# Kernel optimization log

Measured on AMD Instinct MI355X. Metric: run time of the kernel, lower is better.

Reference implementation:

```python
import jax, jax.numpy as jnp
import numpy as np

B, C, H, W = 4, 64, 160, 160
COUT, K = 64, 3
STRIDE, PAD, DIL = 1, 1, 1


def setup_inputs() -> dict:
    key = jax.random.key(0)
    k1, k2, k3, k4, k5 = jax.random.split(key, 5)
    x = jax.random.normal(k1, (B, C, H, W), dtype=jnp.float32)
    # small offset-conv weights -> offsets of O(1) pixel, realistic sampling
    w_off = jax.random.normal(k2, (2 * K * K, C, K, K), dtype=jnp.float32) * 0.01
    b_off = jax.random.normal(k3, (2 * K * K,), dtype=jnp.float32) * 0.01
    weight = jax.random.normal(k4, (COUT, C, K, K), dtype=jnp.float32) / np.sqrt(C * K * K)
    bias = jax.random.normal(k5, (COUT,), dtype=jnp.float32) * 0.01
    return {"x": x, "w_off": w_off, "b_off": b_off, "weight": weight, "bias": bias}


def _deform_conv2d(x, offset, weight, bias):
    """torchvision-style deform_conv2d (v1, groups=1, offset_groups=1)."""
    b, c, h, w = x.shape
    cout, _, k, _ = weight.shape
    kk = k * k
    ho, wo = offset.shape[2], offset.shape[3]
    off = offset.reshape(b, kk, 2, ho, wo)
    dy, dx = off[:, :, 0], off[:, :, 1]  # [B,KK,Ho,Wo]
    # base sampling grid: p0 + kernel offset
    base_y = (jnp.arange(ho) * STRIDE - PAD)[None, :] + (jnp.arange(k) * DIL)[:, None]  # [K,Ho]
    base_x = (jnp.arange(wo) * STRIDE - PAD)[None, :] + (jnp.arange(k) * DIL)[:, None]  # [K,Wo]
    by = jnp.repeat(base_y, k, axis=0)   # [KK,Ho]  (k index = kh*K + kw)
    bx = jnp.tile(base_x, (k, 1))        # [KK,Wo]
    py = by[None, :, :, None] + dy       # [B,KK,Ho,Wo]
    px = bx[None, :, None, :] + dx
    y0 = jnp.floor(py)
    x0 = jnp.floor(px)
    ly = (py - y0)[:, None]              # [B,1,KK,Ho,Wo]
    lx = (px - x0)[:, None]
    y0i = y0.astype(jnp.int32)
    x0i = x0.astype(jnp.int32)
    x_flat = x.reshape(b, c, h * w)

    def gather(yi, xi):
        valid = (yi >= 0) & (yi < h) & (xi >= 0) & (xi < w)
        yc = jnp.clip(yi, 0, h - 1)
        xc = jnp.clip(xi, 0, w - 1)
        lin = (yc * w + xc).reshape(b, 1, -1)
        v = jnp.take_along_axis(x_flat, lin, axis=2).reshape(b, c, kk, ho, wo)
        return v * valid[:, None].astype(x.dtype)

    v00 = gather(y0i, x0i)
    v01 = gather(y0i, x0i + 1)
    v10 = gather(y0i + 1, x0i)
    v11 = gather(y0i + 1, x0i + 1)
    sampled = (v00 * (1 - ly) * (1 - lx) + v01 * (1 - ly) * lx
               + v10 * ly * (1 - lx) + v11 * ly * lx)  # [B,C,KK,Ho,Wo]
    out = jnp.einsum('bckhw,ock->bohw', sampled, weight.reshape(cout, c, kk))
    return out + bias[None, :, None, None]


def reference(x, w_off, b_off, weight, bias):
    offset = jax.lax.conv_general_dilated(
        x, w_off, (STRIDE, STRIDE), ((PAD, PAD), (PAD, PAD)),
        rhs_dilation=(DIL, DIL),
        dimension_numbers=('NCHW', 'OIHW', 'NCHW')) + b_off[None, :, None, None]
    return _deform_conv2d(x, offset, weight, bias)
```

## Files before the change

kernel.cpp:

```cpp
#include <hip/hip_runtime.h>
#include <hip/hip_bf16.h>

#define Bq   4
#define Cc   64
#define Hh   160
#define Ww   160
#define HWp  (Hh * Ww)
#define COUTc 64

typedef __attribute__((ext_vector_type(8))) _Float16 f16x8;
typedef __attribute__((ext_vector_type(4))) _Float16 f16x4;
typedef __attribute__((ext_vector_type(4))) float f32x4;
typedef __attribute__((ext_vector_type(2))) float f32x2;
typedef __attribute__((ext_vector_type(4))) int   int4v;

#define WTBF_SHORTS   (72 * 512)
#define WTOFFF_SHORTS (36 * 512)
#define XCL_OFS       (WTBF_SHORTS + WTOFFF_SHORTS)
#define XCL_PIX       ((size_t)Bq * HWp)
#define XCL_SHORTS    (XCL_PIX * 64 + 64)

#define HROWS 6
#define HCOLS 36
#define HPX   72
#define HSTR  (HCOLS * HPX)

__device__ __forceinline__ short f2h(float f) {
    union { _Float16 h; short s; } v; v.h = (_Float16)f; return v.s;
}
__device__ __forceinline__ unsigned pk2h(float a, float b) {
    union { _Float16 h[2]; unsigned u; } v;
    v.h[0] = (_Float16)a; v.h[1] = (_Float16)b; return v.u;
}
__device__ __forceinline__ f16x8 vsplat(_Float16 v) {
    return (f16x8){v, v, v, v, v, v, v, v};
}

__global__ __launch_bounds__(256) void prep_all(const float* __restrict__ x,
                                                const float* __restrict__ w,
                                                const float* __restrict__ w_off,
                                                short* __restrict__ ws) {
    int blk = blockIdx.x;
    int tid = threadIdx.x;
    if (blk < 400) {
        int g = blk * 256 + tid;
        int b = g / HWp, p = g - b * HWp;
        const float* xp = x + (size_t)b * Cc * HWp + p;
        short* op = ws + XCL_OFS + (size_t)g * 64;
#pragma unroll
        for (int cg = 0; cg < 8; ++cg) {
            unsigned d[4];
#pragma unroll
            for (int dj = 0; dj < 4; ++dj) {
                float f0 = xp[(size_t)(cg * 8 + 2 * dj) * HWp];
                float f1 = xp[(size_t)(cg * 8 + 2 * dj + 1) * HWp];
                d[dj] = pk2h(f0, f1);
            }
            *(int4v*)(op + cg * 8) = *(int4v*)d;
        }
    } else if (blk < 544) {
        int i = (blk - 400) * 256 + tid;
        if (i < WTBF_SHORTS) {
            int fidx = i >> 9, r = i & 511;
            int l = r >> 3, j = r & 7;
            int cg = fidx & 3, th = fidx >> 2;
            int tap = th >> 1, h = th & 1;
            int o = cg * 16 + (l & 15);
            int c = h * 32 + ((l >> 4) << 3) + j;
            ws[i] = f2h(w[o * 576 + c * 9 + tap]);
        }
        if (i < WTOFFF_SHORTS) {
            int fidx = i >> 9, r = i & 511;
            int l = r >> 3, j = r & 7;
            int g = fidx & 1, th = fidx >> 1;
            int tap = th >> 1, h = th & 1;
            int oc = g * 16 + (l & 15);
            int c = h * 32 + ((l >> 4) << 3) + j;
            float v = (oc < 18) ? w_off[oc * 576 + c * 9 + tap] : 0.f;
            ws[WTBF_SHORTS + i] = f2h(v);
        }
    } else {
        if (tid < 8)
            *(int4v*)((char*)(ws + XCL_OFS) + XCL_PIX * 128 + tid * 16) =
                (int4v){0, 0, 0, 0};
    }
}

__global__ __launch_bounds__(256, 4) void fused_cl(const short* __restrict__ ws,
                                                   const float* __restrict__ b_off,
                                                   const float* __restrict__ bias,
                                                   float* __restrict__ out) {
    __shared__ short halo_s[HROWS * HCOLS * HPX];
    __shared__ float offbuf[32][20];
    __shared__ int4v tapT[32][9];

    int tid = threadIdx.x;
    int wid = tid >> 6;
    int l   = tid & 63;
    int lr  = l & 15;
    int lg  = l >> 4;
    int mhalf = wid >> 1;
    int nhalf = wid & 1;

    int bid = blockIdx.x;
    int g_blk = (bid & 7) * 400 + (bid >> 3);

    int pix_base = g_blk * 32;
    int b   = pix_base / HWp;
    int rem = pix_base - b * HWp;
    int y   = rem / Ww;
    int x0  = rem - y * Ww;

    const short* wTbF   = ws;
    const short* wToffF = ws + WTBF_SHORTS;
    const char*  xclb   = (const char*)(ws + XCL_OFS) + (size_t)b * HWp * 128;

    for (int i = tid; i < HROWS * HCOLS * 8; i += 256) {
        int pl = i >> 3, cg2 = i & 7;
        int hy = pl / HCOLS, hx = pl - hy * HCOLS;
        int gy = y - 2 + hy, gx = x0 - 2 + hx;
        int4v v;
        if (gy >= 0 && gy < Hh && gx >= 0 && gx < Ww)
            v = *(const int4v*)(xclb + (size_t)(gy * Ww + gx) * 128 + cg2 * 16);
        else
            v = (int4v){0, 0, 0, 0};
        *(int4v*)(halo_s + pl * HPX + cg2 * 8) = v;
    }
    __syncthreads();

    {
        int hxb = mhalf * 16 + lr + 1;
        int hoffA[9];
#pragma unroll
        for (int t = 0; t < 9; ++t) {
            int ty = t / 3, tx = t - ty * 3;
            hoffA[t] = (ty + 1) * HSTR + (hxb + tx) * HPX + lg * 8;
        }
        const short* wofr = wToffF + (size_t)nhalf * 512 + l * 8;
        f32x4 accA = {0.f, 0.f, 0.f, 0.f};
        f32x4 accB = {0.f, 0.f, 0.f, 0.f};
        f16x8 sB[4];
#pragma unroll
        for (int u = 0; u < 4; ++u)
            sB[u] = *(const f16x8*)(wofr + u * 1024);
        f16x8 sa2[2];
        sa2[0] = *(const f16x8*)(halo_s + hoffA[0]);
#pragma unroll
        for (int u = 0; u < 18; ++u) {
            const int s = u & 3;
            if (u + 1 < 18) {
                const int t2 = (u + 1) >> 1, h2 = (u + 1) & 1;
                sa2[(u + 1) & 1] = *(const f16x8*)(halo_s + hoffA[t2] + h2 * 32);
            }
            if (u & 1)
                accB = __builtin_amdgcn_mfma_f32_16x16x32_f16(sa2[u & 1], sB[s], accB, 0, 0, 0);
            else
                accA = __builtin_amdgcn_mfma_f32_16x16x32_f16(sa2[u & 1], sB[s], accA, 0, 0, 0);
            if (u + 4 < 18)
                sB[s] = *(const f16x8*)(wofr + (u + 4) * 1024);
            __builtin_amdgcn_sched_barrier(0);
        }
        int oc_row = nhalf * 16 + lr;
        if (oc_row < 18) {
            float bv = b_off[oc_row];
#pragma unroll
            for (int j = 0; j < 4; ++j)
                offbuf[mhalf * 16 + lg * 4 + j][oc_row] = accA[j] + accB[j] + bv;
        }
    }
    __syncthreads();

    for (int i = tid; i < 288; i += 256) {
        int px = i / 9, tap = i - px * 9;
        int ty = tap / 3, tx = tap - ty * 3;
        f32x2 d2 = *(const f32x2*)&offbuf[px][2 * tap];
        float py  = (float)(y - 1 + ty) + d2[0];
        float pxf = (float)(x0 + px - 1 + tx) + d2[1];
        float fy = floorf(py), fx = floorf(pxf);
        float ly = py - fy, lx = pxf - fx;
        int iy0 = (int)fy, ix0 = (int)fx;
        int iy1 = iy0 + 1, ix1 = ix0 + 1;
        bool vy0 = (iy0 >= 0) && (iy0 < Hh);
        bool vy1 = (iy1 >= 0) && (iy1 < Hh);
        bool vx0 = (ix0 >= 0) && (ix0 < Ww);
        bool vx1 = (ix1 >= 0) && (ix1 < Ww);
        float w00 = (vy0 && vx0) ? (1.f - ly) * (1.f - lx) : 0.f;
        float w01 = (vy0 && vx1) ? (1.f - ly) * lx         : 0.f;
        float w10 = (vy1 && vx0) ? ly * (1.f - lx)         : 0.f;
        float w11 = (vy1 && vx1) ? ly * lx                 : 0.f;
        int hy = iy0 - (y - 2);
        int hx = ix0 - (x0 - 2);
        bool inH = (hy >= 0) && (hy <= HROWS - 2) && (hx >= 0) && (hx <= HCOLS - 2);
        union { f16x4 h4; int iw[2]; } wu;
        wu.h4 = (f16x4){(_Float16)w00, (_Float16)w01,
                        (_Float16)w10, (_Float16)w11};
        int4v tv;
        tv[0] = inH ? (hy * HSTR + hx * HPX) : -1;
        tv[1] = (iy0 & 0xffff) | (ix0 << 16);
        tv[2] = wu.iw[0];
        tv[3] = wu.iw[1];
        tapT[px][tap] = tv;
    }
    __syncthreads();

    f32x4 acc[2];
    acc[0] = (f32x4){0.f, 0.f, 0.f, 0.f};
    acc[1] = (f32x4){0.f, 0.f, 0.f, 0.f};
    int px_t = mhalf * 16 + lr;
    const short* wfb = wTbF + (size_t)nhalf * 1024 + l * 8;

    f16x8 sB0[2], sB1[2];
    sB0[0] = *(const f16x8*)(wfb);
    sB1[0] = *(const f16x8*)(wfb + 512);
    sB0[1] = *(const f16x8*)(wfb + 2048);
    sB1[1] = *(const f16x8*)(wfb + 2048 + 512);

    int4v tp[2];
    tp[0] = tapT[px_t][0];
    tp[1] = tapT[px_t][1];

    f16x8 cst[2][8];
    {
        const short* q = halo_s + max(tp[0][0], 0) + lg * 8;
#pragma unroll
        for (int h = 0; h < 2; ++h) {
            const short* qh = q + h * 32;
            cst[0][h * 4 + 0] = *(const f16x8*)(qh);
            cst[0][h * 4 + 1] = *(const f16x8*)(qh + HPX);
            cst[0][h * 4 + 2] = *(const f16x8*)(qh + HSTR);
            cst[0][h * 4 + 3] = *(const f16x8*)(qh + HSTR + HPX);
        }
    }

#pragma unroll
    for (int t = 0; t < 9; ++t) {
        const int cur = t & 1, nx = cur ^ 1;

        const int ho = tp[cur][0];
        const int fb = tp[cur][1];
        union { int iw[2]; f16x4 h4; } wu;
        wu.iw[0] = tp[cur][2];
        wu.iw[1] = tp[cur][3];
        f16x4 wg = wu.h4;

        if (t + 2 < 9)
            tp[cur] = tapT[px_t][t + 2];

        if (t < 8) {
            const short* q = halo_s + max(tp[nx][0], 0) + lg * 8;
#pragma unroll
            for (int h = 0; h < 2; ++h) {
                const short* qh = q + h * 32;
                cst[nx][h * 4 + 0] = *(const f16x8*)(qh);
                cst[nx][h * 4 + 1] = *(const f16x8*)(qh + HPX);
                cst[nx][h * 4 + 2] = *(const f16x8*)(qh + HSTR);
                cst[nx][h * 4 + 3] = *(const f16x8*)(qh + HSTR + HPX);
            }
        }
        __builtin_amdgcn_sched_barrier(0);

#pragma unroll
        for (int h = 0; h < 2; ++h) {
            const int u = 2 * t + h, s = u & 1;
            f16x8 a = cst[cur][h * 4 + 0] * vsplat(wg[0])
                    + cst[cur][h * 4 + 1] * vsplat(wg[1])
                    + cst[cur][h * 4 + 2] * vsplat(wg[2])
                    + cst[cur][h * 4 + 3] * vsplat(wg[3]);
            if (ho < 0) {
                int iy0 = (int)(short)(fb & 0xffff);
                int ix0 = fb >> 16;
                int cy0 = min(max(iy0, 0), Hh - 1), cy1 = min(max(iy0 + 1, 0), Hh - 1);
                int cx0 = min(max(ix0, 0), Ww - 1), cx1 = min(max(ix0 + 1, 0), Ww - 1);
                int cbh = h * 64 + lg * 16;
                f16x8 g00 = *(const f16x8*)(xclb + (size_t)(cy0 * Ww + cx0) * 128 + cbh);
                f16x8 g01 = *(const f16x8*)(xclb + (size_t)(cy0 * Ww + cx1) * 128 + cbh);
                f16x8 g10 = *(const f16x8*)(xclb + (size_t)(cy1 * Ww + cx0) * 128 + cbh);
                f16x8 g11 = *(const f16x8*)(xclb + (size_t)(cy1 * Ww + cx1) * 128 + cbh);
                a = g00 * vsplat(wg[0]) + g01 * vsplat(wg[1])
                  + g10 * vsplat(wg[2]) + g11 * vsplat(wg[3]);
            }
            acc[0] = __builtin_amdgcn_mfma_f32_16x16x32_f16(a, sB0[s], acc[0], 0, 0, 0);
            acc[1] = __builtin_amdgcn_mfma_f32_16x16x32_f16(a, sB1[s], acc[1], 0, 0, 0);
            if (u + 2 < 18) {
                sB0[s] = *(const f16x8*)(wfb + (u + 2) * 2048);
                sB1[s] = *(const f16x8*)(wfb + (u + 2) * 2048 + 512);
            }
        }
        __builtin_amdgcn_sched_barrier(0);
    }

    float* obase = out + (size_t)b * COUTc * HWp + y * Ww + x0;
#pragma unroll
    for (int nt = 0; nt < 2; ++nt) {
        int o = nhalf * 32 + nt * 16 + lr;
        float bv = bias[o];
#pragma unroll
        for (int j = 0; j < 4; ++j)
            obase[(size_t)o * HWp + mhalf * 16 + lg * 4 + j] = acc[nt][j] + bv;
    }
}

extern "C" void kernel_launch(void* const* d_in, const int* in_sizes, int n_in,
                              void* d_out, int out_size, void* d_ws, size_t ws_size,
                              hipStream_t stream) {
    const float* x      = (const float*)d_in[0];
    const float* w_off  = (const float*)d_in[1];
    const float* b_off  = (const float*)d_in[2];
    const float* weight = (const float*)d_in[3];
    const float* bias   = (const float*)d_in[4];
    float* outp = (float*)d_out;
    short* ws   = (short*)d_ws;

    prep_all<<<545, 256, 0, stream>>>(x, weight, w_off, ws);

    int nblocks = (Bq * HWp) / 32;
    fused_cl<<<nblocks, 256, 0, stream>>>(ws, b_off, bias, outp);
}
```

Baseline: 53.06 us.

## Process 2x32 pixel tiles per block with each wave covering all output channels

Each block now handles two output rows of 32 pixels instead of one row, so the halo grows from 6 to 7 rows and is shared by twice as many pixels, which cuts the halo-load overhead per pixel. Each wave now computes 16 pixels across all 64 output channels (and both offset-channel tiles) rather than splitting channels between waves. This removes the duplicated bilinear sampling work that the old channel split caused. The costs are more registers per thread, more LDS per block, and a lower occupancy hint (3 blocks instead of 4). The block count is halved and the grid index swizzle is adjusted to match.

Result: faster. 49.65 us (median of 3 runs) (-6.4%).

```diff
diff --git a/kernel.cpp b/kernel.cpp
--- a/kernel.cpp
+++ b/kernel.cpp
@@ -20,7 +20,7 @@
 #define XCL_PIX       ((size_t)Bq * HWp)
 #define XCL_SHORTS    (XCL_PIX * 64 + 64)
 
-#define HROWS 6
+#define HROWS 7
 #define HCOLS 36
 #define HPX   72
 #define HSTR  (HCOLS * HPX)
@@ -86,30 +86,29 @@
     }
 }
 
-__global__ __launch_bounds__(256, 4) void fused_cl(const short* __restrict__ ws,
+__global__ __launch_bounds__(256, 3) void fused_cl(const short* __restrict__ ws,
                                                    const float* __restrict__ b_off,
                                                    const float* __restrict__ bias,
                                                    float* __restrict__ out) {
     __shared__ short halo_s[HROWS * HCOLS * HPX];
-    __shared__ float offbuf[32][20];
-    __shared__ int4v tapT[32][9];
+    __shared__ float offbuf[64][20];
+    __shared__ int4v tapT[64][9];
 
     int tid = threadIdx.x;
     int wid = tid >> 6;
     int l   = tid & 63;
     int lr  = l & 15;
     int lg  = l >> 4;
-    int mhalf = wid >> 1;
-    int nhalf = wid & 1;
 
     int bid = blockIdx.x;
-    int g_blk = (bid & 7) * 400 + (bid >> 3);
-
-    int pix_base = g_blk * 32;
-    int b   = pix_base / HWp;
-    int rem = pix_base - b * HWp;
-    int y   = rem / Ww;
-    int x0  = rem - y * Ww;
+    int g_blk = (bid & 7) * 200 + (bid >> 3);
+
+    int b  = g_blk / 400;
+    int r  = g_blk - b * 400;
+    int ty2 = r / 5;
+    int tx2 = r - ty2 * 5;
+    int y  = ty2 * 2;
+    int x0 = tx2 * 32;
 
     const short* wTbF   = ws;
     const short* wToffF = ws + WTBF_SHORTS;
@@ -129,53 +128,61 @@
     __syncthreads();
 
     {
-        int hxb = mhalf * 16 + lr + 1;
+        int rowoff = wid >> 1;
+        int colw   = (wid & 1) * 16 + lr;
+        int hxb    = colw + 1;
         int hoffA[9];
 #pragma unroll
         for (int t = 0; t < 9; ++t) {
             int ty = t / 3, tx = t - ty * 3;
-            hoffA[t] = (ty + 1) * HSTR + (hxb + tx) * HPX + lg * 8;
-        }
-        const short* wofr = wToffF + (size_t)nhalf * 512 + l * 8;
-        f32x4 accA = {0.f, 0.f, 0.f, 0.f};
-        f32x4 accB = {0.f, 0.f, 0.f, 0.f};
-        f16x8 sB[4];
-#pragma unroll
-        for (int u = 0; u < 4; ++u)
-            sB[u] = *(const f16x8*)(wofr + u * 1024);
+            hoffA[t] = (rowoff + ty + 1) * HSTR + (hxb + tx) * HPX + lg * 8;
+        }
+        const short* wofr = wToffF + l * 8;
+        f32x4 accO0 = {0.f, 0.f, 0.f, 0.f};
+        f32x4 accO1 = {0.f, 0.f, 0.f, 0.f};
+        f16x8 sB0[4], sB1[4];
+#pragma unroll
+        for (int u = 0; u < 4; ++u) {
+            sB0[u] = *(const f16x8*)(wofr + u * 1024);
+            sB1[u] = *(const f16x8*)(wofr + u * 1024 + 512);
+        }
         f16x8 sa2[2];
         sa2[0] = *(const f16x8*)(halo_s + hoffA[0]);
 #pragma unroll
         for (int u = 0; u < 18; ++u) {
-            const int s = u & 3;
+            const int s4 = u & 3;
             if (u + 1 < 18) {
                 const int t2 = (u + 1) >> 1, h2 = (u + 1) & 1;
                 sa2[(u + 1) & 1] = *(const f16x8*)(halo_s + hoffA[t2] + h2 * 32);
             }
-            if (u & 1)
-                accB = __builtin_amdgcn_mfma_f32_16x16x32_f16(sa2[u & 1], sB[s], accB, 0, 0, 0);
-            else
-                accA = __builtin_amdgcn_mfma_f32_16x16x32_f16(sa2[u & 1], sB[s], accA, 0, 0, 0);
-            if (u + 4 < 18)
-                sB[s] = *(const f16x8*)(wofr + (u + 4) * 1024);
+            accO0 = __builtin_amdgcn_mfma_f32_16x16x32_f16(sa2[u & 1], sB0[s4], accO0, 0, 0, 0);
+            accO1 = __builtin_amdgcn_mfma_f32_16x16x32_f16(sa2[u & 1], sB1[s4], accO1, 0, 0, 0);
+            if (u + 4 < 18) {
+                sB0[s4] = *(const f16x8*)(wofr + (u + 4) * 1024);
+                sB1[s4] = *(const f16x8*)(wofr + (u + 4) * 1024 + 512);
+            }
             __builtin_amdgcn_sched_barrier(0);
         }
-        int oc_row = nhalf * 16 + lr;
-        if (oc_row < 18) {
-            float bv = b_off[oc_row];
+        float bv0 = b_off[lr];
+#pragma unroll
+        for (int j = 0; j < 4; ++j)
+            offbuf[wid * 16 + lg * 4 + j][lr] = accO0[j] + bv0;
+        if (lr < 2) {
+            float bv1 = b_off[16 + lr];
 #pragma unroll
             for (int j = 0; j < 4; ++j)
-                offbuf[mhalf * 16 + lg * 4 + j][oc_row] = accA[j] + accB[j] + bv;
+                offbuf[wid * 16 + lg * 4 + j][16 + lr] = accO1[j] + bv1;
         }
     }
     __syncthreads();
 
-    for (int i = tid; i < 288; i += 256) {
+    for (int i = tid; i < 576; i += 256) {
         int px = i / 9, tap = i - px * 9;
+        int prow = px >> 5, pcol = px & 31;
         int ty = tap / 3, tx = tap - ty * 3;
         f32x2 d2 = *(const f32x2*)&offbuf[px][2 * tap];
-        float py  = (float)(y - 1 + ty) + d2[0];
-        float pxf = (float)(x0 + px - 1 + tx) + d2[1];
+        float py  = (float)(y + prow - 1 + ty) + d2[0];
+        float pxf = (float)(x0 + pcol - 1 + tx) + d2[1];
         float fy = floorf(py), fx = floorf(pxf);
         float ly = py - fy, lx = pxf - fx;
         int iy0 = (int)fy, ix0 = (int)fx;
@@ -203,21 +210,22 @@
     }
     __syncthreads();
 
-    f32x4 acc[2];
-    acc[0] = (f32x4){0.f, 0.f, 0.f, 0.f};
-    acc[1] = (f32x4){0.f, 0.f, 0.f, 0.f};
-    int px_t = mhalf * 16 + lr;
-    const short* wfb = wTbF + (size_t)nhalf * 1024 + l * 8;
-
-    f16x8 sB0[2], sB1[2];
-    sB0[0] = *(const f16x8*)(wfb);
-    sB1[0] = *(const f16x8*)(wfb + 512);
-    sB0[1] = *(const f16x8*)(wfb + 2048);
-    sB1[1] = *(const f16x8*)(wfb + 2048 + 512);
+    f32x4 acc[4];
+#pragma unroll
+    for (int cg = 0; cg < 4; ++cg) acc[cg] = (f32x4){0.f, 0.f, 0.f, 0.f};
+    int px3 = wid * 16 + lr;
+    const short* wfb = wTbF + l * 8;
+
+    f16x8 sBc[2][4];
+#pragma unroll
+    for (int cg = 0; cg < 4; ++cg) {
+        sBc[0][cg] = *(const f16x8*)(wfb + (0 * 4 + cg) * 512);
+        sBc[1][cg] = *(const f16x8*)(wfb + (1 * 4 + cg) * 512);
+    }
 
     int4v tp[2];
-    tp[0] = tapT[px_t][0];
-    tp[1] = tapT[px_t][1];
+    tp[0] = tapT[px3][0];
+    tp[1] = tapT[px3][1];
 
     f16x8 cst[2][8];
     {
@@ -244,7 +252,7 @@
         f16x4 wg = wu.h4;
 
         if (t + 2 < 9)
-            tp[cur] = tapT[px_t][t + 2];
+            tp[cur] = tapT[px3][t + 2];
 
         if (t < 8) {
             const short* q = halo_s + max(tp[nx][0], 0) + lg * 8;
@@ -279,11 +287,14 @@
                 a = g00 * vsplat(wg[0]) + g01 * vsplat(wg[1])
                   + g10 * vsplat(wg[2]) + g11 * vsplat(wg[3]);
             }
-            acc[0] = __builtin_amdgcn_mfma_f32_16x16x32_f16(a, sB0[s], acc[0], 0, 0, 0);
-            acc[1] = __builtin_amdgcn_mfma_f32_16x16x32_f16(a, sB1[s], acc[1], 0, 0, 0);
+            acc[0] = __builtin_amdgcn_mfma_f32_16x16x32_f16(a, sBc[s][0], acc[0], 0, 0, 0);
+            acc[1] = __builtin_amdgcn_mfma_f32_16x16x32_f16(a, sBc[s][1], acc[1], 0, 0, 0);
+            acc[2] = __builtin_amdgcn_mfma_f32_16x16x32_f16(a, sBc[s][2], acc[2], 0, 0, 0);
+            acc[3] = __builtin_amdgcn_mfma_f32_16x16x32_f16(a, sBc[s][3], acc[3], 0, 0, 0);
             if (u + 2 < 18) {
-                sB0[s] = *(const f16x8*)(wfb + (u + 2) * 2048);
-                sB1[s] = *(const f16x8*)(wfb + (u + 2) * 2048 + 512);
+#pragma unroll
+                for (int cg = 0; cg < 4; ++cg)
+                    sBc[s][cg] = *(const f16x8*)(wfb + ((u + 2) * 4 + cg) * 512);
             }
         }
         __builtin_amdgcn_sched_barrier(0);
@@ -291,12 +302,15 @@
 
     float* obase = out + (size_t)b * COUTc * HWp + y * Ww + x0;
 #pragma unroll
-    for (int nt = 0; nt < 2; ++nt) {
-        int o = nhalf * 32 + nt * 16 + lr;
+    for (int cg = 0; cg < 4; ++cg) {
+        int o = cg * 16 + lr;
         float bv = bias[o];
 #pragma unroll
-        for (int j = 0; j < 4; ++j)
-            obase[(size_t)o * HWp + mhalf * 16 + lg * 4 + j] = acc[nt][j] + bv;
+        for (int j = 0; j < 4; ++j) {
+            int px = wid * 16 + lg * 4 + j;
+            int prow = px >> 5, pcol = px & 31;
+            obase[(size_t)o * HWp + prow * Ww + pcol] = acc[cg][j] + bv;
+        }
     }
 }
 
@@ -313,6 +327,6 @@
 
     prep_all<<<545, 256, 0, stream>>>(x, weight, w_off, ws);
 
-    int nblocks = (Bq * HWp) / 32;
+    int nblocks = (Bq * HWp) / 64;
     fused_cl<<<nblocks, 256, 0, stream>>>(ws, b_off, bias, outp);
 }
```
